# Performance work log

Hardware: AMD Instinct MI355X
Metric: run time of the kernel (lower is better)

## Reference

```python
import jax, jax.numpy as jnp
import numpy as np

B, DIM, NUM_HEADS = 16384, 2048, 4
SD = DIM // 2            # single_dim = 1024
HD = SD // NUM_HEADS     # head_dim = 256
LH = SD // 4             # lambda-net hidden = 256
SCALE = HD ** -0.5


def setup_inputs() -> dict:
    key = jax.random.key(0)
    ks = jax.random.split(key, 20)
    w = lambda k, shape: jax.random.normal(k, shape, dtype=jnp.float32) * 0.02
    inp = {
        "x": jax.random.normal(ks[0], (B, DIM), dtype=jnp.float32),
        # Linear weights stored (in, out); y = x @ W + b (equivalent to torch Linear)
        "WQ1_w": w(ks[1], (SD, SD)), "WQ1_b": jnp.zeros((SD,), jnp.float32),
        "WK1_w": w(ks[2], (SD, SD)), "WK1_b": jnp.zeros((SD,), jnp.float32),
        "WQ2_w": w(ks[3], (SD, SD)), "WQ2_b": jnp.zeros((SD,), jnp.float32),
        "WK2_w": w(ks[4], (SD, SD)), "WK2_b": jnp.zeros((SD,), jnp.float32),
        "WV_w": w(ks[5], (SD, SD)), "WV_b": jnp.zeros((SD,), jnp.float32),
        "WO_w": w(ks[6], (SD, SD)), "WO_b": jnp.zeros((SD,), jnp.float32),
        "L1_w": w(ks[7], (DIM, LH)), "L1_b": jnp.zeros((LH,), jnp.float32),
        "L2_w": w(ks[8], (LH, 1)), "L2_b": jnp.zeros((1,), jnp.float32),
    }
    return inp


def _heads(t, W, b):
    # tokens [B,2,SD] -> [B,H,2,HD]
    y = t @ W + b
    return y.reshape(B, 2, NUM_HEADS, HD).transpose(0, 2, 1, 3)


def reference(x, WQ1_w, WQ1_b, WK1_w, WK1_b, WQ2_w, WQ2_b, WK2_w, WK2_b,
              WV_w, WV_b, WO_w, WO_b, L1_w, L1_b, L2_w, L2_b):
    tokens = x.reshape(B, 2, SD)
    # gating lambda in (0,1): MLP(x) -> [B,1,1,1]
    lam = jax.nn.sigmoid(jax.nn.relu(x @ L1_w + L1_b) @ L2_w + L2_b)
    lam = lam.reshape(B, 1, 1, 1)

    Q1 = _heads(tokens, WQ1_w, WQ1_b)
    K1 = _heads(tokens, WK1_w, WK1_b)
    Q2 = _heads(tokens, WQ2_w, WQ2_b)
    K2 = _heads(tokens, WK2_w, WK2_b)
    V = _heads(tokens, WV_w, WV_b)

    attn1 = jax.nn.softmax(jnp.einsum("bhqd,bhkd->bhqk", Q1, K1) * SCALE, axis=-1)
    attn2 = jax.nn.softmax(jnp.einsum("bhqd,bhkd->bhqk", Q2, K2) * SCALE, axis=-1)
    diff_attn = jax.nn.relu(attn1 - lam * attn2)  # dropout = identity (eval)

    out = jnp.einsum("bhqk,bhkd->bhqd", diff_attn, V)  # [B,H,2,HD]
    out = out.transpose(0, 2, 1, 3).reshape(B, 2, SD)
    out = (out @ WO_w + WO_b) + tokens
    return out.reshape(B, SD * 2)
```

## Files before the change

kernel.cpp:

```cpp
#include <hip/hip_runtime.h>
#include <stdint.h>


#define BATCH  16384
#define ATT_SCALE 0.0625f

typedef __attribute__((ext_vector_type(8)))  short   s16x8;
typedef __attribute__((ext_vector_type(4)))  float   f32x4;
typedef __attribute__((ext_vector_type(2)))  float   f32x2;
typedef __attribute__((ext_vector_type(8)))  int     i32x8;
typedef __attribute__((ext_vector_type(8)))  unsigned short u16x8;
typedef __attribute__((ext_vector_type(4)))  unsigned short u16x4;

__device__ __forceinline__ unsigned short f2bf(float f) {
  unsigned u = __float_as_uint(f);
  u += 0x7FFFu + ((u >> 16) & 1u);
  return (unsigned short)(u >> 16);
}
__device__ __forceinline__ float bf2f(unsigned short s) {
  return __uint_as_float((unsigned)s << 16);
}

__device__ __forceinline__ unsigned char f2e4m3(float f) {
  unsigned u = __float_as_uint(f);
  unsigned s = (u >> 24) & 0x80u;
  float a = fabsf(f);
  if (a >= 448.f) return (unsigned char)(s | 0x7E);
  if (a < 0.0009765625f) return (unsigned char)s;
  int e = (int)((u >> 23) & 0xFF) - 127;
  if (e < -6) {
    int q = (int)rintf(a * 512.f);
    if (q >= 8) return (unsigned char)(s | 0x08);
    return (unsigned char)(s | q);
  }
  unsigned mant = u & 0x7FFFFFu;
  unsigned mr = mant + 0x7FFFFu + ((mant >> 20) & 1u);
  e += (int)(mr >> 23);
  mant = (mr >> 20) & 7u;
  if (e > 8) return (unsigned char)(s | 0x7E);
  return (unsigned char)(s | ((e + 7) << 3) | mant);
}
__device__ __forceinline__ float e4m3f(unsigned v) {
  unsigned e = (v >> 3) & 15u, m = v & 7u;
  float mag = (e == 0) ? (float)m * 0.001953125f
                       : __uint_as_float(((e + 120u) << 23) | (m << 20));
  return (v & 0x80u) ? -mag : mag;
}

__device__ __forceinline__ unsigned char cvt1_fp8(float v) {
#if __has_builtin(__builtin_amdgcn_cvt_pk_fp8_f32)
  return (unsigned char)(__builtin_amdgcn_cvt_pk_fp8_f32(v, v, 0, false) & 0xff);
#else
  return f2e4m3(v);
#endif
}

__device__ __forceinline__ void dec8(uint2 p, float* o) {
#if __has_builtin(__builtin_amdgcn_cvt_pk_f32_fp8)
  f32x2 a = __builtin_amdgcn_cvt_pk_f32_fp8((int)p.x, false);
  f32x2 b = __builtin_amdgcn_cvt_pk_f32_fp8((int)p.x, true);
  f32x2 c = __builtin_amdgcn_cvt_pk_f32_fp8((int)p.y, false);
  f32x2 d = __builtin_amdgcn_cvt_pk_f32_fp8((int)p.y, true);
  o[0] = a[0]; o[1] = a[1]; o[2] = b[0]; o[3] = b[1];
  o[4] = c[0]; o[5] = c[1]; o[6] = d[0]; o[7] = d[1];
#else
#pragma unroll
  for (int j = 0; j < 4; ++j) o[j]     = e4m3f((p.x >> (8 * j)) & 255u);
#pragma unroll
  for (int j = 0; j < 4; ++j) o[4 + j] = e4m3f((p.y >> (8 * j)) & 255u);
#endif
}

__device__ __forceinline__ void async16(const void* g, void* l) {
  __builtin_amdgcn_global_load_lds((__attribute__((address_space(1))) void*)g,
                                   (__attribute__((address_space(3))) void*)l,
                                   16, 0, 0);
}

__global__ __launch_bounds__(512, 2)
void gemm_mx(const unsigned char* __restrict__ A,
             const unsigned char* __restrict__ Bt,
             const float* __restrict__ bias,
             unsigned char* __restrict__ Cout,
             unsigned short* __restrict__ Vout,
             int NN,
             const unsigned short* __restrict__ xbf,
             const unsigned short* __restrict__ lamBt,
             const float* __restrict__ lamL1b,
             const float* __restrict__ lamL2w,
             float* __restrict__ lamp)
{
  __shared__ __align__(16) char lds[131072];
  const int tid  = threadIdx.x;
  const int lane = tid & 63, w = tid >> 6;
  const int wm = w >> 2, wn = w & 3;
  const int li = lane & 15, lc = lane >> 4;

  if (blockIdx.x < 128) {
    const int bm_l = blockIdx.x * 128;
    const int t = tid;
    const size_t aSrc  = (size_t)(bm_l + (t >> 2)) * 2048 + (t & 3) * 8;
    const size_t b0Src = (size_t)(t >> 2) * 2048 + (t & 3) * 8;
    const size_t b1Src = (size_t)(128 + (t >> 2)) * 2048 + (t & 3) * 8;

    f32x4 acc[4][4];
#pragma unroll
    for (int i = 0; i < 4; ++i)
#pragma unroll
      for (int j = 0; j < 4; ++j) acc[i][j] = (f32x4)0.f;

    for (int k0 = 0; k0 < 2048; k0 += 32) {
      async16(xbf   + aSrc  + k0, lds + w * 1024);
      async16(lamBt + b0Src + k0, lds + 8192 + w * 1024);
      async16(lamBt + b1Src + k0, lds + 16384 + w * 1024);
      __syncthreads();
      s16x8 aR[4], bR[4];
#pragma unroll
      for (int m = 0; m < 4; ++m)
        aR[m] = *(const s16x8*)(lds + ((w >> 2) * 64 + m * 16 + li) * 64 + lc * 16);
#pragma unroll
      for (int n = 0; n < 4; ++n)
        bR[n] = *(const s16x8*)(lds + 8192 + ((w & 3) * 64 + n * 16 + li) * 64 + lc * 16);
#pragma unroll
      for (int m = 0; m < 4; ++m)
#pragma unroll
        for (int n = 0; n < 4; ++n)
          acc[m][n] = __builtin_amdgcn_mfma_f32_16x16x32_bf16(aR[m], bR[n], acc[m][n], 0, 0, 0);
      __syncthreads();
    }

    float l2v[4], bvv[4];
#pragma unroll
    for (int n = 0; n < 4; ++n) {
      const int col = (w & 3) * 64 + n * 16 + li;
      l2v[n] = lamL2w[col];
      bvv[n] = lamL1b[col];
    }
#pragma unroll
    for (int m = 0; m < 4; ++m)
#pragma unroll
      for (int j = 0; j < 4; ++j) {
        float part = 0.f;
#pragma unroll
        for (int n = 0; n < 4; ++n)
          part += fmaxf(acc[m][n][j] + bvv[n], 0.f) * l2v[n];
        part += __shfl_xor(part, 1, 64);
        part += __shfl_xor(part, 2, 64);
        part += __shfl_xor(part, 4, 64);
        part += __shfl_xor(part, 8, 64);
        if ((lane & 15) == 0)
          atomicAdd(lamp + bm_l + (w >> 2) * 64 + m * 16 + lc * 4 + j, part);
      }
    return;
  }

  const int bid = blockIdx.x - 128;
  const int nwg = 2560;
  const int swz = (bid & 7) * (nwg >> 3) + (bid >> 3);
  const int bm = (swz / NN) * 256;
  const int bn = (swz % NN) * 256;

  const int grow   = lane >> 3;
  const int gchunk = ((lane & 7) ^ grow) * 16;
  size_t aSrc[4], bSrc[4];
  int dstKB[4];
#pragma unroll
  for (int i = 0; i < 4; ++i) {
    const int rr = (i * 8 + w) * 8 + grow;
    aSrc[i] = (size_t)(bm + rr) * 1024 + gchunk;
    bSrc[i] = (size_t)(bn + rr) * 1024 + gchunk;
    dstKB[i] = (i * 8 + w) * 1024;
  }

  const int x7   = li & 7;
  const int off0 = ((2 * lc)     ^ x7) * 16;
  const int off1 = ((2 * lc + 1) ^ x7) * 16;
  const int aRow = (wm * 128 + li) * 128;
  const int bRow = 32768 + (wn * 64 + li) * 128;

  f32x4 acc[8][4];
#pragma unroll
  for (int m = 0; m < 8; ++m)
#pragma unroll
    for (int n = 0; n < 4; ++n) acc[m][n] = (f32x4)0.f;

#pragma unroll
  for (int i = 0; i < 4; ++i) {
    async16(A  + aSrc[i], lds + dstKB[i]);
    async16(Bt + bSrc[i], lds + 32768 + dstKB[i]);
  }
#pragma unroll
  for (int i = 0; i < 4; ++i) {
    async16(A  + aSrc[i] + 128, lds + 65536 + dstKB[i]);
    async16(Bt + bSrc[i] + 128, lds + 98304 + dstKB[i]);
  }
  asm volatile("s_waitcnt vmcnt(8)" ::: "memory");
  __builtin_amdgcn_s_barrier();

  for (int t = 0; t < 8; ++t) {
    char* buf = lds + (t & 1) * 65536;

    i32x8 bF[4];
#pragma unroll
    for (int nf = 0; nf < 4; ++nf) {
      const char* p = buf + bRow + nf * 2048;
      uint4 h0 = *(const uint4*)(p + off0);
      uint4 h1 = *(const uint4*)(p + off1);
      bF[nf][0] = h0.x; bF[nf][1] = h0.y; bF[nf][2] = h0.z; bF[nf][3] = h0.w;
      bF[nf][4] = h1.x; bF[nf][5] = h1.y; bF[nf][6] = h1.z; bF[nf][7] = h1.w;
    }
#pragma unroll
    for (int mh = 0; mh < 2; ++mh) {
      i32x8 aF[4];
#pragma unroll
      for (int mf = 0; mf < 4; ++mf) {
        const char* p = buf + aRow + (mh * 4 + mf) * 2048;
        uint4 h0 = *(const uint4*)(p + off0);
        uint4 h1 = *(const uint4*)(p + off1);
        aF[mf][0] = h0.x; aF[mf][1] = h0.y; aF[mf][2] = h0.z; aF[mf][3] = h0.w;
        aF[mf][4] = h1.x; aF[mf][5] = h1.y; aF[mf][6] = h1.z; aF[mf][7] = h1.w;
      }
      __builtin_amdgcn_s_setprio(1);
#pragma unroll
      for (int mf = 0; mf < 4; ++mf)
#pragma unroll
        for (int nf = 0; nf < 4; ++nf)
          acc[mh * 4 + mf][nf] = __builtin_amdgcn_mfma_scale_f32_16x16x128_f8f6f4(
              aF[mf], bF[nf], acc[mh * 4 + mf][nf],
              0, 0, 0, 0x7F7F7F7F, 0, 0x7F7F7F7F);
      __builtin_amdgcn_s_setprio(0);
    }
    __builtin_amdgcn_s_barrier();
    if (t + 2 < 8) {
      const size_t kt = (size_t)(t + 2) * 128;
#pragma unroll
      for (int i = 0; i < 4; ++i) {
        async16(A  + aSrc[i] + kt, buf + dstKB[i]);
        async16(Bt + bSrc[i] + kt, buf + 32768 + dstKB[i]);
      }
    }
    if (t < 6) { asm volatile("s_waitcnt vmcnt(8)" ::: "memory"); }
    else       { asm volatile("s_waitcnt vmcnt(0)" ::: "memory"); }
    __builtin_amdgcn_s_barrier();
  }

  float bv[4];
#pragma unroll
  for (int n = 0; n < 4; ++n) bv[n] = bias[bn + wn * 64 + n * 16 + li];

  if (bn < 4096) {
    unsigned char* wl0 = (unsigned char*)(lds + w * 12288);
#pragma unroll
    for (int mp = 0; mp < 4; ++mp) {
      unsigned char* wl = wl0 + (mp & 1) * 2560;
#pragma unroll
      for (int mi = 0; mi < 2; ++mi)
#pragma unroll
        for (int n = 0; n < 4; ++n)
#pragma unroll
          for (int jj = 0; jj < 4; ++jj) {
            float v = acc[mp * 2 + mi][n][jj] + bv[n];
            wl[(mi * 16 + lc * 4 + jj) * 80 + n * 16 + li] = cvt1_fp8(v);
          }
      const size_t base = (size_t)((bm + wm * 128 + mp * 32) >> 5) * 131072
                        + (size_t)((bn >> 6) + wn) * 2048;
      uint4 v0 = *(const uint4*)(wl + (lane >> 2) * 80 + (lane & 3) * 16);
      *(uint4*)(Cout + base + lane * 16) = v0;
      uint4 v1 = *(const uint4*)(wl + (16 + (lane >> 2)) * 80 + (lane & 3) * 16);
      *(uint4*)(Cout + base + 1024 + lane * 16) = v1;
    }
  } else {
    unsigned short* wl0 = (unsigned short*)(lds + w * 12288);
    const int cb = bn - 4096;
#pragma unroll
    for (int mp = 0; mp < 4; ++mp) {
      unsigned short* wl = wl0 + (mp & 1) * 2304;
#pragma unroll
      for (int mi = 0; mi < 2; ++mi)
#pragma unroll
        for (int n = 0; n < 4; ++n)
#pragma unroll
          for (int jj = 0; jj < 4; ++jj) {
            float v = acc[mp * 2 + mi][n][jj] + bv[n];
            wl[(mi * 16 + lc * 4 + jj) * 72 + li + n * 16] = f2bf(v);
          }
#pragma unroll
      for (int i = 0; i < 4; ++i) {
        const int rr = i * 8 + (lane >> 3);
        u16x8 vv = *(const u16x8*)(wl + rr * 72 + (lane & 7) * 8);
        const size_t gi = (size_t)(bm + wm * 128 + mp * 32 + rr) * 1024
                        + cb + wn * 64 + (lane & 7) * 8;
        *(u16x8*)(Vout + gi) = vv;
      }
    }
  }
}

__global__ __launch_bounds__(512, 2)
void gemm_wo(const unsigned short* __restrict__ A,
             const unsigned short* __restrict__ Bt,
             const float* __restrict__ bias,
             float* __restrict__ Cout,
             const unsigned short* __restrict__ res,
             int Kdim, int Ndim, int NN)
{
  __shared__ __align__(16) char lds[131072];
  const int tid  = threadIdx.x;
  const int lane = tid & 63, w = tid >> 6;
  const int wm = w >> 2, wn = w & 3;
  const int li = lane & 15, lc = lane >> 4;

  const int nwg = gridDim.x;
  const int q8 = nwg >> 3, r8 = nwg & 7;
  const int xcd = blockIdx.x & 7, pos = blockIdx.x >> 3;
  const int swz = (xcd < r8 ? xcd * (q8 + 1) : r8 * (q8 + 1) + (xcd - r8) * q8) + pos;
  const int bm = (swz / NN) * 256;
  const int bn = (swz % NN) * 256;

  const int r0  = w * 32 + (lane >> 2);
  const int csw = ((lane & 3) ^ ((r0 >> 1) & 3)) * 8;
  const size_t aS0 = (size_t)(bm + r0) * Kdim + csw;
  const size_t aS1 = (size_t)(bm + r0 + 16) * Kdim + csw;
  const size_t bS0 = (size_t)(bn + r0) * Kdim + csw;
  const size_t bS1 = (size_t)(bn + r0 + 16) * Kdim + csw;
  const int dL0 = w * 2048, dL1 = dL0 + 1024;

  const int fsw   = (lc ^ ((li >> 1) & 3)) << 4;
  const int afoff = (wm * 128 + li) * 64 + fsw;
  const int bfoff = 32768 + (wn * 64 + li) * 64 + fsw;

  f32x4 acc[8][4];
#pragma unroll
  for (int m = 0; m < 8; ++m)
#pragma unroll
    for (int n = 0; n < 4; ++n) acc[m][n] = (f32x4)0.f;

  const int NT = Kdim >> 6;

  async16(A  + aS0,       lds + dL0);          async16(A  + aS1,       lds + dL1);
  async16(Bt + bS0,       lds + 32768 + dL0);  async16(Bt + bS1,       lds + 32768 + dL1);
  async16(A  + aS0 + 32,  lds + 16384 + dL0);  async16(A  + aS1 + 32,  lds + 16384 + dL1);
  async16(Bt + bS0 + 32,  lds + 49152 + dL0);  async16(Bt + bS1 + 32,  lds + 49152 + dL1);
  async16(A  + aS0 + 64,  lds + 65536 + dL0);  async16(A  + aS1 + 64,  lds + 65536 + dL1);
  async16(Bt + bS0 + 64,  lds + 98304 + dL0);  async16(Bt + bS1 + 64,  lds + 98304 + dL1);
  asm volatile("s_waitcnt vmcnt(4)" ::: "memory");
  __builtin_amdgcn_s_barrier();

  for (int t = 0; t < NT; ++t) {
    char* buf  = lds + (t & 1) * 65536;
    char* nbuf = lds + ((t + 1) & 1) * 65536;
    const size_t kA = (size_t)t * 64;
    const bool s1 = (t + 1 < NT), s2 = (t + 2 < NT);
    s16x8 a0[4], a1[4], bR[4];

    {
      const char* ab = buf + afoff;
      const char* bb = buf + bfoff;
#pragma unroll
      for (int i = 0; i < 4; ++i) a0[i] = *(const s16x8*)(ab + i * 1024);
#pragma unroll
      for (int i = 0; i < 4; ++i) a1[i] = *(const s16x8*)(ab + 4096 + i * 1024);
#pragma unroll
      for (int i = 0; i < 4; ++i) bR[i] = *(const s16x8*)(bb + i * 1024);
      if (s1) {
        async16(A  + aS0 + kA + 96, nbuf + 16384 + dL0);
        async16(A  + aS1 + kA + 96, nbuf + 16384 + dL1);
        async16(Bt + bS0 + kA + 96, nbuf + 49152 + dL0);
        async16(Bt + bS1 + kA + 96, nbuf + 49152 + dL1);
      }
      __builtin_amdgcn_s_setprio(1);
#pragma unroll
      for (int mf = 0; mf < 4; ++mf)
#pragma unroll
        for (int nf = 0; nf < 4; ++nf) {
          acc[mf][nf]     = __builtin_amdgcn_mfma_f32_16x16x32_bf16(a0[mf], bR[nf], acc[mf][nf], 0, 0, 0);
          acc[4 + mf][nf] = __builtin_amdgcn_mfma_f32_16x16x32_bf16(a1[mf], bR[nf], acc[4 + mf][nf], 0, 0, 0);
        }
      __builtin_amdgcn_s_setprio(0);
      __builtin_amdgcn_s_barrier();
    }
    {
      const char* ab = buf + 16384 + afoff;
      const char* bb = buf + 16384 + bfoff;
#pragma unroll
      for (int i = 0; i < 4; ++i) a0[i] = *(const s16x8*)(ab + i * 1024);
#pragma unroll
      for (int i = 0; i < 4; ++i) a1[i] = *(const s16x8*)(ab + 4096 + i * 1024);
#pragma unroll
      for (int i = 0; i < 4; ++i) bR[i] = *(const s16x8*)(bb + i * 1024);
      if (s2) {
        async16(A  + aS0 + kA + 128, buf + dL0);
        async16(A  + aS1 + kA + 128, buf + dL1);
        async16(Bt + bS0 + kA + 128, buf + 32768 + dL0);
        async16(Bt + bS1 + kA + 128, buf + 32768 + dL1);
      }
      __builtin_amdgcn_s_setprio(1);
#pragma unroll
      for (int mf = 0; mf < 4; ++mf)
#pragma unroll
        for (int nf = 0; nf < 4; ++nf) {
          acc[mf][nf]     = __builtin_amdgcn_mfma_f32_16x16x32_bf16(a0[mf], bR[nf], acc[mf][nf], 0, 0, 0);
          acc[4 + mf][nf] = __builtin_amdgcn_mfma_f32_16x16x32_bf16(a1[mf], bR[nf], acc[4 + mf][nf], 0, 0, 0);
        }
      __builtin_amdgcn_s_setprio(0);
      if (t < NT - 2)       { asm volatile("s_waitcnt vmcnt(4)" ::: "memory"); }
      else if (t == NT - 2) { asm volatile("s_waitcnt vmcnt(0)" ::: "memory"); }
      __builtin_amdgcn_s_barrier();
    }
  }

  float bv[4];
#pragma unroll
  for (int n = 0; n < 4; ++n) bv[n] = bias[bn + wn * 64 + n * 16 + li];

  float* wl0 = (float*)(lds + w * 12288);
#pragma unroll
  for (int m = 0; m < 8; ++m) {
    float* wl = wl0 + (m & 1) * 1088;
#pragma unroll
    for (int n = 0; n < 4; ++n)
#pragma unroll
      for (int jj = 0; jj < 4; ++jj)
        wl[(lc * 4 + jj) * 68 + li + n * 16] = acc[m][n][jj] + bv[n];
#pragma unroll
    for (int i = 0; i < 4; ++i) {
      const int rr = i * 4 + lc;
      f32x4 vv = *(const f32x4*)(wl + rr * 68 + li * 4);
      const size_t gi = (size_t)(bm + wm * 128 + m * 16 + rr) * Ndim
                      + bn + wn * 64 + li * 4;
      const u16x4 rv = *(const u16x4*)(res + gi);
      f32x4 ov;
#pragma unroll
      for (int jj = 0; jj < 4; ++jj) ov[jj] = vv[jj] + bf2f(rv[jj]);
      *(f32x4*)(Cout + gi) = ov;
    }
  }
}

__global__ __launch_bounds__(256)
void attn_kernel(const unsigned char* __restrict__ qk8,
                 const unsigned short* __restrict__ vbuf,
                 const float* __restrict__ lam_pre,
                 const float* __restrict__ L2b,
                 unsigned short* __restrict__ aout)
{
  const int b = blockIdx.x;
  const int hd = threadIdx.x >> 6;
  const int lane = threadIdx.x & 63;
  const int g = lane >> 5;
  const int l5 = lane & 31;
  const size_t row = (size_t)(2 * b + g);

  const size_t cbase = (row >> 5) * 131072
                     + (size_t)(hd * 4 + (l5 >> 3)) * 2048
                     + (row & 31) * 64 + (l5 & 7) * 8;
  const uint2 p1 = *(const uint2*)(qk8 + cbase);
  const uint2 p2 = *(const uint2*)(qk8 + cbase + 32768);
  const uint2 p3 = *(const uint2*)(qk8 + cbase + 65536);
  const uint2 p4 = *(const uint2*)(qk8 + cbase + 98304);
  const u16x8 vvv = *(const u16x8*)(vbuf + row * 1024 + hd * 256 + l5 * 8);

  float q1[8], k1[8], q2[8], k2[8], vf[8];
  dec8(p1, q1); dec8(p2, k1); dec8(p3, q2); dec8(p4, k2);
#pragma unroll
  for (int j = 0; j < 8; ++j) vf[j] = bf2f(vvv[j]);

  float ss1 = 0.f, sc1 = 0.f, ss2 = 0.f, sc2 = 0.f;
#pragma unroll
  for (int j = 0; j < 8; ++j) {
    const float k1o = __shfl_xor(k1[j], 32, 64);
    const float k2o = __shfl_xor(k2[j], 32, 64);
    ss1 += q1[j] * k1[j]; sc1 += q1[j] * k1o;
    ss2 += q2[j] * k2[j]; sc2 += q2[j] * k2o;
  }
#pragma unroll
  for (int m = 16; m >= 1; m >>= 1) {
    ss1 += __shfl_xor(ss1, m, 64); sc1 += __shfl_xor(sc1, m, 64);
    ss2 += __shfl_xor(ss2, m, 64); sc2 += __shfl_xor(sc2, m, 64);
  }

  float e0 = ss1 * ATT_SCALE, e1 = sc1 * ATT_SCALE;
  float mx = fmaxf(e0, e1);
  float xs = expf(e0 - mx), xc = expf(e1 - mx);
  float inv = 1.f / (xs + xc);
  const float a1s = xs * inv, a1c = xc * inv;

  e0 = ss2 * ATT_SCALE; e1 = sc2 * ATT_SCALE;
  mx = fmaxf(e0, e1);
  xs = expf(e0 - mx); xc = expf(e1 - mx);
  inv = 1.f / (xs + xc);
  const float a2s = xs * inv, a2c = xc * inv;

  const float lm = 1.f / (1.f + expf(-(lam_pre[b] + L2b[0])));
  const float ps = fmaxf(a1s - lm * a2s, 0.f);
  const float pc = fmaxf(a1c - lm * a2c, 0.f);

  u16x8 o;
#pragma unroll
  for (int j = 0; j < 8; ++j) {
    const float vo = __shfl_xor(vf[j], 32, 64);
    o[j] = f2bf(ps * vf[j] + pc * vo);
  }
  *(u16x8*)(aout + row * 1024 + hd * 256 + l5 * 8) = o;
}

__global__ void prep_k(const float* __restrict__ s0, const float* __restrict__ s1,
                       const float* __restrict__ s2, const float* __restrict__ s3,
                       const float* __restrict__ s4, const float* __restrict__ s5,
                       const float* __restrict__ L1w,
                       const float* __restrict__ b0, const float* __restrict__ b1,
                       const float* __restrict__ b2, const float* __restrict__ b3,
                       const float* __restrict__ b4,
                       const float* __restrict__ x,
                       unsigned char* __restrict__ qw8,
                       unsigned short* __restrict__ wot,
                       unsigned short* __restrict__ l1t,
                       float* __restrict__ bcat,
                       unsigned short* __restrict__ x_bf,
                       unsigned char* __restrict__ x_f8,
                       float* __restrict__ lamp)
{
  __shared__ float tile[32][33];
  const int z = blockIdx.z;
  const int tx = threadIdx.x, ty = threadIdx.y;

  if (z < 6) {
    const float* W;
    switch (z) {
      case 0: W = s0; break;
      case 1: W = s1; break;
      case 2: W = s2; break;
      case 3: W = s3; break;
      case 4: W = s4; break;
      default: W = s5; break;
    }
    const int bn = blockIdx.x * 32, bk = blockIdx.y * 32;
#pragma unroll
    for (int i = ty; i < 32; i += 8)
      tile[i][tx] = W[(size_t)(bk + i) * 1024 + bn + tx];
    __syncthreads();
    if (z < 5) {
      unsigned char* Wt = qw8 + (size_t)z * 1048576;
#pragma unroll
      for (int i = ty; i < 32; i += 8)
        Wt[(size_t)(bn + i) * 1024 + bk + tx] = cvt1_fp8(tile[tx][i]);
    } else {
#pragma unroll
      for (int i = ty; i < 32; i += 8)
        wot[(size_t)(bn + i) * 1024 + bk + tx] = f2bf(tile[tx][i]);
    }
    return;
  }
  if (z < 22) {
    const int c = (z - 6) * 1024 + blockIdx.y * 32 + blockIdx.x;
    const int i = c * 256 + ty * 32 + tx;
    const float4* p = (const float4*)x + (size_t)i * 2;
    float4 a = p[0], b = p[1];
    float f[8] = {a.x, a.y, a.z, a.w, b.x, b.y, b.z, b.w};
    u16x8 v; unsigned lo = 0, hi = 0;
#pragma unroll
    for (int j = 0; j < 8; ++j) v[j] = f2bf(f[j]);
#pragma unroll
    for (int j = 0; j < 4; ++j) lo |= (unsigned)cvt1_fp8(f[j]) << (8 * j);
#pragma unroll
    for (int j = 0; j < 4; ++j) hi |= (unsigned)cvt1_fp8(f[4 + j]) << (8 * j);
    *(u16x8*)(x_bf + (size_t)i * 8) = v;
    uint2 c8; c8.x = lo; c8.y = hi;
    *(uint2*)(x_f8 + (size_t)i * 8) = c8;
    return;
  }
  if (z == 22) {
    const int idx = blockIdx.y * 32 + blockIdx.x;
    if (idx >= 512) return;
    const int bn = (idx & 7) * 32, bk = (idx >> 3) * 32;
#pragma unroll
    for (int i = ty; i < 32; i += 8)
      tile[i][tx] = L1w[(size_t)(bk + i) * 256 + bn + tx];
    __syncthreads();
#pragma unroll
    for (int i = ty; i < 32; i += 8)
      l1t[(size_t)(bn + i) * 2048 + bk + tx] = f2bf(tile[tx][i]);
    return;
  }
  const int idx = blockIdx.y * 32 + blockIdx.x;
  const int t = ty * 32 + tx;
  if (idx < 20) {
    const int i = idx * 256 + t;
    const float* src;
    switch (i >> 10) {
      case 0: src = b0; break;
      case 1: src = b1; break;
      case 2: src = b2; break;
      case 3: src = b3; break;
      default: src = b4; break;
    }
    bcat[i] = src[i & 1023];
  } else if (idx < 84) {
    lamp[(idx - 20) * 256 + t] = 0.f;
  }
}

extern "C" void kernel_launch(void* const* d_in, const int* in_sizes, int n_in,
                              void* d_out, int out_size, void* d_ws, size_t ws_size,
                              hipStream_t stream)
{
  const float* x    = (const float*)d_in[0];
  const float* WQ1w = (const float*)d_in[1];  const float* WQ1b = (const float*)d_in[2];
  const float* WK1w = (const float*)d_in[3];  const float* WK1b = (const float*)d_in[4];
  const float* WQ2w = (const float*)d_in[5];  const float* WQ2b = (const float*)d_in[6];
  const float* WK2w = (const float*)d_in[7];  const float* WK2b = (const float*)d_in[8];
  const float* WVw  = (const float*)d_in[9];  const float* WVb  = (const float*)d_in[10];
  const float* WOw  = (const float*)d_in[11]; const float* WOb  = (const float*)d_in[12];
  const float* L1w  = (const float*)d_in[13]; const float* L1b  = (const float*)d_in[14];
  const float* L2w  = (const float*)d_in[15]; const float* L2b  = (const float*)d_in[16];

  char* ws = (char*)d_ws;
  size_t off = 0;
  unsigned short* x_bf = (unsigned short*)(ws + off); off += (size_t)33554432 * 2;
  unsigned char*  x_f8 = (unsigned char*)(ws + off);  off += (size_t)33554432;
  unsigned char*  qw8  = (unsigned char*)(ws + off);  off += (size_t)5242880;
  unsigned short* wot  = (unsigned short*)(ws + off); off += (size_t)1048576 * 2;
  unsigned short* l1t  = (unsigned short*)(ws + off); off += (size_t)524288 * 2;
  float*          bcat = (float*)(ws + off);          off += (size_t)5120 * 4;
  unsigned char*  qk8  = (unsigned char*)(ws + off);  off += (size_t)32768 * 4096;
  unsigned short* vbuf = (unsigned short*)(ws + off); off += (size_t)33554432 * 2;
  unsigned short* abuf = (unsigned short*)(ws + off); off += (size_t)33554432 * 2;
  float*          lamp = (float*)(ws + off);          off += (size_t)16384 * 4;

  prep_k<<<dim3(32, 32, 24), dim3(32, 8), 0, stream>>>(
      WQ1w, WK1w, WQ2w, WK2w, WVw, WOw, L1w,
      WQ1b, WK1b, WQ2b, WK2b, WVb, x,
      qw8, wot, l1t, bcat, x_bf, x_f8, lamp);

  gemm_mx<<<dim3(128 + 2560), 512, 0, stream>>>(
      x_f8, qw8, bcat, qk8, vbuf, 20, x_bf, l1t, L1b, L2w, lamp);

  attn_kernel<<<16384, 256, 0, stream>>>(qk8, vbuf, lamp, L2b, abuf);

  gemm_wo<<<dim3(512), 512, 0, stream>>>(
      abuf, wot, WOb, (float*)d_out, x_bf, 1024, 1024, 4);
}
```

Before: 428.7 us.

## Run output projection GEMM in FP8 MX-scaled MFMA instead of bf16

The attention output and WO weights are now stored as FP8 e4m3, and the WO GEMM uses the 16x16x128 f8f6f4 scaled MFMA with unit scales and a 128-byte K-tile pipeline. This halves the bytes read for the attention buffer and weights and raises matrix throughput per instruction. It also packs four FP8 epilogue bytes into one 32-bit LDS store in the QKV GEMM. The cost is extra quantization error in the output projection.

```diff
diff --git a/kernel.cpp b/kernel.cpp
--- a/kernel.cpp
+++ b/kernel.cpp
@@ -256,12 +256,15 @@
 #pragma unroll
       for (int mi = 0; mi < 2; ++mi)
 #pragma unroll
-        for (int n = 0; n < 4; ++n)
-#pragma unroll
-          for (int jj = 0; jj < 4; ++jj) {
+        for (int jj = 0; jj < 4; ++jj) {
+          unsigned d = 0;
+#pragma unroll
+          for (int n = 0; n < 4; ++n) {
             float v = acc[mp * 2 + mi][n][jj] + bv[n];
-            wl[(mi * 16 + lc * 4 + jj) * 80 + n * 16 + li] = cvt1_fp8(v);
+            d |= (unsigned)cvt1_fp8(v) << (8 * n);
           }
+          *(unsigned*)(wl + (mi * 16 + lc * 4 + jj) * 80 + li * 4) = d;
+        }
       const size_t base = (size_t)((bm + wm * 128 + mp * 32) >> 5) * 131072
                         + (size_t)((bn >> 6) + wn) * 2048;
       uint4 v0 = *(const uint4*)(wl + (lane >> 2) * 80 + (lane & 3) * 16);
@@ -297,12 +300,11 @@
 }
 
 __global__ __launch_bounds__(512, 2)
-void gemm_wo(const unsigned short* __restrict__ A,
-             const unsigned short* __restrict__ Bt,
-             const float* __restrict__ bias,
-             float* __restrict__ Cout,
-             const unsigned short* __restrict__ res,
-             int Kdim, int Ndim, int NN)
+void gemm_womx(const unsigned char* __restrict__ A,
+               const unsigned char* __restrict__ Bt,
+               const float* __restrict__ bias,
+               float* __restrict__ Cout,
+               const unsigned short* __restrict__ res)
 {
   __shared__ __align__(16) char lds[131072];
   const int tid  = threadIdx.x;
@@ -310,24 +312,27 @@
   const int wm = w >> 2, wn = w & 3;
   const int li = lane & 15, lc = lane >> 4;
 
-  const int nwg = gridDim.x;
-  const int q8 = nwg >> 3, r8 = nwg & 7;
-  const int xcd = blockIdx.x & 7, pos = blockIdx.x >> 3;
-  const int swz = (xcd < r8 ? xcd * (q8 + 1) : r8 * (q8 + 1) + (xcd - r8) * q8) + pos;
-  const int bm = (swz / NN) * 256;
-  const int bn = (swz % NN) * 256;
-
-  const int r0  = w * 32 + (lane >> 2);
-  const int csw = ((lane & 3) ^ ((r0 >> 1) & 3)) * 8;
-  const size_t aS0 = (size_t)(bm + r0) * Kdim + csw;
-  const size_t aS1 = (size_t)(bm + r0 + 16) * Kdim + csw;
-  const size_t bS0 = (size_t)(bn + r0) * Kdim + csw;
-  const size_t bS1 = (size_t)(bn + r0 + 16) * Kdim + csw;
-  const int dL0 = w * 2048, dL1 = dL0 + 1024;
-
-  const int fsw   = (lc ^ ((li >> 1) & 3)) << 4;
-  const int afoff = (wm * 128 + li) * 64 + fsw;
-  const int bfoff = 32768 + (wn * 64 + li) * 64 + fsw;
+  const int swz = (blockIdx.x & 7) * 64 + (blockIdx.x >> 3);
+  const int bm = (swz >> 2) * 256;
+  const int bn = (swz & 3) * 256;
+
+  const int grow   = lane >> 3;
+  const int gchunk = ((lane & 7) ^ grow) * 16;
+  size_t aSrc[4], bSrc[4];
+  int dstKB[4];
+#pragma unroll
+  for (int i = 0; i < 4; ++i) {
+    const int rr = (i * 8 + w) * 8 + grow;
+    aSrc[i] = (size_t)(bm + rr) * 1024 + gchunk;
+    bSrc[i] = (size_t)(bn + rr) * 1024 + gchunk;
+    dstKB[i] = (i * 8 + w) * 1024;
+  }
+
+  const int x7   = li & 7;
+  const int off0 = ((2 * lc)     ^ x7) * 16;
+  const int off1 = ((2 * lc + 1) ^ x7) * 16;
+  const int aRow = (wm * 128 + li) * 128;
+  const int bRow = 32768 + (wn * 64 + li) * 128;
 
   f32x4 acc[8][4];
 #pragma unroll
@@ -335,78 +340,64 @@
 #pragma unroll
     for (int n = 0; n < 4; ++n) acc[m][n] = (f32x4)0.f;
 
-  const int NT = Kdim >> 6;
-
-  async16(A  + aS0,       lds + dL0);          async16(A  + aS1,       lds + dL1);
-  async16(Bt + bS0,       lds + 32768 + dL0);  async16(Bt + bS1,       lds + 32768 + dL1);
-  async16(A  + aS0 + 32,  lds + 16384 + dL0);  async16(A  + aS1 + 32,  lds + 16384 + dL1);
-  async16(Bt + bS0 + 32,  lds + 49152 + dL0);  async16(Bt + bS1 + 32,  lds + 49152 + dL1);
-  async16(A  + aS0 + 64,  lds + 65536 + dL0);  async16(A  + aS1 + 64,  lds + 65536 + dL1);
-  async16(Bt + bS0 + 64,  lds + 98304 + dL0);  async16(Bt + bS1 + 64,  lds + 98304 + dL1);
-  asm volatile("s_waitcnt vmcnt(4)" ::: "memory");
+#pragma unroll
+  for (int i = 0; i < 4; ++i) {
+    async16(A  + aSrc[i], lds + dstKB[i]);
+    async16(Bt + bSrc[i], lds + 32768 + dstKB[i]);
+  }
+#pragma unroll
+  for (int i = 0; i < 4; ++i) {
+    async16(A  + aSrc[i] + 128, lds + 65536 + dstKB[i]);
+    async16(Bt + bSrc[i] + 128, lds + 98304 + dstKB[i]);
+  }
+  asm volatile("s_waitcnt vmcnt(8)" ::: "memory");
   __builtin_amdgcn_s_barrier();
 
-  for (int t = 0; t < NT; ++t) {
-    char* buf  = lds + (t & 1) * 65536;
-    char* nbuf = lds + ((t + 1) & 1) * 65536;
-    const size_t kA = (size_t)t * 64;
-    const bool s1 = (t + 1 < NT), s2 = (t + 2 < NT);
-    s16x8 a0[4], a1[4], bR[4];
-
-    {
-      const char* ab = buf + afoff;
-      const char* bb = buf + bfoff;
-#pragma unroll
-      for (int i = 0; i < 4; ++i) a0[i] = *(const s16x8*)(ab + i * 1024);
-#pragma unroll
-      for (int i = 0; i < 4; ++i) a1[i] = *(const s16x8*)(ab + 4096 + i * 1024);
-#pragma unroll
-      for (int i = 0; i < 4; ++i) bR[i] = *(const s16x8*)(bb + i * 1024);
-      if (s1) {
-        async16(A  + aS0 + kA + 96, nbuf + 16384 + dL0);
-        async16(A  + aS1 + kA + 96, nbuf + 16384 + dL1);
-        async16(Bt + bS0 + kA + 96, nbuf + 49152 + dL0);
-        async16(Bt + bS1 + kA + 96, nbuf + 49152 + dL1);
+  for (int t = 0; t < 8; ++t) {
+    char* buf = lds + (t & 1) * 65536;
+
+    i32x8 bF[4];
+#pragma unroll
+    for (int nf = 0; nf < 4; ++nf) {
+      const char* p = buf + bRow + nf * 2048;
+      uint4 h0 = *(const uint4*)(p + off0);
+      uint4 h1 = *(const uint4*)(p + off1);
+      bF[nf][0] = h0.x; bF[nf][1] = h0.y; bF[nf][2] = h0.z; bF[nf][3] = h0.w;
+      bF[nf][4] = h1.x; bF[nf][5] = h1.y; bF[nf][6] = h1.z; bF[nf][7] = h1.w;
+    }
+#pragma unroll
+    for (int mh = 0; mh < 2; ++mh) {
+      i32x8 aF[4];
+#pragma unroll
+      for (int mf = 0; mf < 4; ++mf) {
+        const char* p = buf + aRow + (mh * 4 + mf) * 2048;
+        uint4 h0 = *(const uint4*)(p + off0);
+        uint4 h1 = *(const uint4*)(p + off1);
+        aF[mf][0] = h0.x; aF[mf][1] = h0.y; aF[mf][2] = h0.z; aF[mf][3] = h0.w;
+        aF[mf][4] = h1.x; aF[mf][5] = h1.y; aF[mf][6] = h1.z; aF[mf][7] = h1.w;
       }
       __builtin_amdgcn_s_setprio(1);
 #pragma unroll
       for (int mf = 0; mf < 4; ++mf)
 #pragma unroll
-        for (int nf = 0; nf < 4; ++nf) {
-          acc[mf][nf]     = __builtin_amdgcn_mfma_f32_16x16x32_bf16(a0[mf], bR[nf], acc[mf][nf], 0, 0, 0);
-          acc[4 + mf][nf] = __builtin_amdgcn_mfma_f32_16x16x32_bf16(a1[mf], bR[nf], acc[4 + mf][nf], 0, 0, 0);
-        }
+        for (int nf = 0; nf < 4; ++nf)
+          acc[mh * 4 + mf][nf] = __builtin_amdgcn_mfma_scale_f32_16x16x128_f8f6f4(
+              aF[mf], bF[nf], acc[mh * 4 + mf][nf],
+              0, 0, 0, 0x7F7F7F7F, 0, 0x7F7F7F7F);
       __builtin_amdgcn_s_setprio(0);
-      __builtin_amdgcn_s_barrier();
-    }
-    {
-      const char* ab = buf + 16384 + afoff;
-      const char* bb = buf + 16384 + bfoff;
-#pragma unroll
-      for (int i = 0; i < 4; ++i) a0[i] = *(const s16x8*)(ab + i * 1024);
-#pragma unroll
-      for (int i = 0; i < 4; ++i) a1[i] = *(const s16x8*)(ab + 4096 + i * 1024);
-#pragma unroll
-      for (int i = 0; i < 4; ++i) bR[i] = *(const s16x8*)(bb + i * 1024);
-      if (s2) {
-        async16(A  + aS0 + kA + 128, buf + dL0);
-        async16(A  + aS1 + kA + 128, buf + dL1);
-        async16(Bt + bS0 + kA + 128, buf + 32768 + dL0);
-        async16(Bt + bS1 + kA + 128, buf + 32768 + dL1);
+    }
+    __builtin_amdgcn_s_barrier();
+    if (t + 2 < 8) {
+      const size_t kt = (size_t)(t + 2) * 128;
+#pragma unroll
+      for (int i = 0; i < 4; ++i) {
+        async16(A  + aSrc[i] + kt, buf + dstKB[i]);
+        async16(Bt + bSrc[i] + kt, buf + 32768 + dstKB[i]);
       }
-      __builtin_amdgcn_s_setprio(1);
-#pragma unroll
-      for (int mf = 0; mf < 4; ++mf)
-#pragma unroll
-        for (int nf = 0; nf < 4; ++nf) {
-          acc[mf][nf]     = __builtin_amdgcn_mfma_f32_16x16x32_bf16(a0[mf], bR[nf], acc[mf][nf], 0, 0, 0);
-          acc[4 + mf][nf] = __builtin_amdgcn_mfma_f32_16x16x32_bf16(a1[mf], bR[nf], acc[4 + mf][nf], 0, 0, 0);
-        }
-      __builtin_amdgcn_s_setprio(0);
-      if (t < NT - 2)       { asm volatile("s_waitcnt vmcnt(4)" ::: "memory"); }
-      else if (t == NT - 2) { asm volatile("s_waitcnt vmcnt(0)" ::: "memory"); }
-      __builtin_amdgcn_s_barrier();
-    }
+    }
+    if (t < 6) { asm volatile("s_waitcnt vmcnt(8)" ::: "memory"); }
+    else       { asm volatile("s_waitcnt vmcnt(0)" ::: "memory"); }
+    __builtin_amdgcn_s_barrier();
   }
 
   float bv[4];
@@ -426,7 +417,7 @@
     for (int i = 0; i < 4; ++i) {
       const int rr = i * 4 + lc;
       f32x4 vv = *(const f32x4*)(wl + rr * 68 + li * 4);
-      const size_t gi = (size_t)(bm + wm * 128 + m * 16 + rr) * Ndim
+      const size_t gi = (size_t)(bm + wm * 128 + m * 16 + rr) * 1024
                       + bn + wn * 64 + li * 4;
       const u16x4 rv = *(const u16x4*)(res + gi);
       f32x4 ov;
@@ -442,7 +433,7 @@
                  const unsigned short* __restrict__ vbuf,
                  const float* __restrict__ lam_pre,
                  const float* __restrict__ L2b,
-                 unsigned short* __restrict__ aout)
+                 unsigned char* __restrict__ aout8)
 {
   const int b = blockIdx.x;
   const int hd = threadIdx.x >> 6;
@@ -495,13 +486,19 @@
   const float ps = fmaxf(a1s - lm * a2s, 0.f);
   const float pc = fmaxf(a1c - lm * a2c, 0.f);
 
-  u16x8 o;
-#pragma unroll
-  for (int j = 0; j < 8; ++j) {
+  unsigned lo = 0, hi = 0;
+#pragma unroll
+  for (int j = 0; j < 4; ++j) {
     const float vo = __shfl_xor(vf[j], 32, 64);
-    o[j] = f2bf(ps * vf[j] + pc * vo);
-  }
-  *(u16x8*)(aout + row * 1024 + hd * 256 + l5 * 8) = o;
+    lo |= (unsigned)cvt1_fp8(ps * vf[j] + pc * vo) << (8 * j);
+  }
+#pragma unroll
+  for (int j = 4; j < 8; ++j) {
+    const float vo = __shfl_xor(vf[j], 32, 64);
+    hi |= (unsigned)cvt1_fp8(ps * vf[j] + pc * vo) << (8 * (j - 4));
+  }
+  uint2 o2; o2.x = lo; o2.y = hi;
+  *(uint2*)(aout8 + row * 1024 + hd * 256 + l5 * 8) = o2;
 }
 
 __global__ void prep_k(const float* __restrict__ s0, const float* __restrict__ s1,
@@ -513,7 +510,7 @@
                        const float* __restrict__ b4,
                        const float* __restrict__ x,
                        unsigned char* __restrict__ qw8,
-                       unsigned short* __restrict__ wot,
+                       unsigned char* __restrict__ wot8,
                        unsigned short* __restrict__ l1t,
                        float* __restrict__ bcat,
                        unsigned short* __restrict__ x_bf,
@@ -539,16 +536,10 @@
     for (int i = ty; i < 32; i += 8)
       tile[i][tx] = W[(size_t)(bk + i) * 1024 + bn + tx];
     __syncthreads();
-    if (z < 5) {
-      unsigned char* Wt = qw8 + (size_t)z * 1048576;
-#pragma unroll
-      for (int i = ty; i < 32; i += 8)
-        Wt[(size_t)(bn + i) * 1024 + bk + tx] = cvt1_fp8(tile[tx][i]);
-    } else {
-#pragma unroll
-      for (int i = ty; i < 32; i += 8)
-        wot[(size_t)(bn + i) * 1024 + bk + tx] = f2bf(tile[tx][i]);
-    }
+    unsigned char* Wt = (z < 5) ? (qw8 + (size_t)z * 1048576) : wot8;
+#pragma unroll
+    for (int i = ty; i < 32; i += 8)
+      Wt[(size_t)(bn + i) * 1024 + bk + tx] = cvt1_fp8(tile[tx][i]);
     return;
   }
   if (z < 22) {
@@ -616,27 +607,27 @@
 
   char* ws = (char*)d_ws;
   size_t off = 0;
-  unsigned short* x_bf = (unsigned short*)(ws + off); off += (size_t)33554432 * 2;
-  unsigned char*  x_f8 = (unsigned char*)(ws + off);  off += (size_t)33554432;
-  unsigned char*  qw8  = (unsigned char*)(ws + off);  off += (size_t)5242880;
-  unsigned short* wot  = (unsigned short*)(ws + off); off += (size_t)1048576 * 2;
-  unsigned short* l1t  = (unsigned short*)(ws + off); off += (size_t)524288 * 2;
-  float*          bcat = (float*)(ws + off);          off += (size_t)5120 * 4;
-  unsigned char*  qk8  = (unsigned char*)(ws + off);  off += (size_t)32768 * 4096;
-  unsigned short* vbuf = (unsigned short*)(ws + off); off += (size_t)33554432 * 2;
-  unsigned short* abuf = (unsigned short*)(ws + off); off += (size_t)33554432 * 2;
-  float*          lamp = (float*)(ws + off);          off += (size_t)16384 * 4;
+  unsigned short* x_bf  = (unsigned short*)(ws + off); off += (size_t)33554432 * 2;
+  unsigned char*  x_f8  = (unsigned char*)(ws + off);  off += (size_t)33554432;
+  unsigned char*  qw8   = (unsigned char*)(ws + off);  off += (size_t)5242880;
+  unsigned char*  wot8  = (unsigned char*)(ws + off);  off += (size_t)1048576;
+  unsigned short* l1t   = (unsigned short*)(ws + off); off += (size_t)524288 * 2;
+  float*          bcat  = (float*)(ws + off);          off += (size_t)5120 * 4;
+  unsigned char*  qk8   = (unsigned char*)(ws + off);  off += (size_t)32768 * 4096;
+  unsigned short* vbuf  = (unsigned short*)(ws + off); off += (size_t)33554432 * 2;
+  unsigned char*  abuf8 = (unsigned char*)(ws + off);  off += (size_t)33554432;
+  float*          lamp  = (float*)(ws + off);          off += (size_t)16384 * 4;
 
   prep_k<<<dim3(32, 32, 24), dim3(32, 8), 0, stream>>>(
       WQ1w, WK1w, WQ2w, WK2w, WVw, WOw, L1w,
       WQ1b, WK1b, WQ2b, WK2b, WVb, x,
-      qw8, wot, l1t, bcat, x_bf, x_f8, lamp);
+      qw8, wot8, l1t, bcat, x_bf, x_f8, lamp);
 
   gemm_mx<<<dim3(128 + 2560), 512, 0, stream>>>(
       x_f8, qw8, bcat, qk8, vbuf, 20, x_bf, l1t, L1b, L2w, lamp);
 
-  attn_kernel<<<16384, 256, 0, stream>>>(qk8, vbuf, lamp, L2b, abuf);
-
-  gemm_wo<<<dim3(512), 512, 0, stream>>>(
-      abuf, wot, WOb, (float*)d_out, x_bf, 1024, 1024, 4);
-}
+  attn_kernel<<<16384, 256, 0, stream>>>(qk8, vbuf, lamp, L2b, abuf8);
+
+  gemm_womx<<<dim3(512), 512, 0, stream>>>(
+      abuf8, wot8, WOb, (float*)d_out, x_bf);
+}
```

Result: faster. 399.1 us (-6.9%).
